# Kernel tuning notes

Hardware: AMD Instinct MI355X
Metric: run time of the kernel (lower is better)

The kernel has to match this reference:

```python
import jax, jax.numpy as jnp
import numpy as np

N, M, D, DV = 8192, 8192, 128, 128

def setup_inputs() -> dict:
    key = jax.random.key(0)
    kq, kk, kv = jax.random.split(key, 3)
    return {
        "Q": jax.random.normal(kq, (N, D), dtype=jnp.float32),
        "K": jax.random.normal(kk, (M, D), dtype=jnp.float32),
        "V": jax.random.normal(kv, (M, DV), dtype=jnp.float32),
    }

def reference(Q, K, V):
    # scores: [N, M] = Q @ K^T (no 1/sqrt(d) scaling, matching the source)
    scores = jnp.einsum("nd,md->nm", Q, K)
    attention_weights = jax.nn.softmax(scores, axis=1)  # softmax over keys
    return jnp.einsum("nm,mv->nv", attention_weights, V)  # [N, DV]
```

## Files before the change

kernel.cpp:

```cpp
#include <hip/hip_runtime.h>
#include <hip/hip_bf16.h>

#define NQ   8192
#define NKEY 8192
#define DH   128

#define BQ   128
#define BK   64
#define BUFB 32768
#define LOG2E 1.44269504088896340736f

typedef __attribute__((ext_vector_type(8)))  short    short8;
typedef __attribute__((ext_vector_type(4)))  short    short4v;
typedef _Float16 half8 __attribute__((ext_vector_type(8)));
typedef __attribute__((ext_vector_type(16))) float    f32x16;
typedef __attribute__((ext_vector_type(4)))  float    float4v;

union BFU { __hip_bfloat16 b; unsigned short u; };
__device__ __forceinline__ unsigned short f2bf(float x) { BFU u; u.b = __float2bfloat16(x); return u.u; }

__device__ __forceinline__ void full_drain_barrier() {
    __builtin_amdgcn_s_waitcnt(0);
    __syncthreads();
}

__global__ void prep(const float* __restrict__ K, const float* __restrict__ V,
                     _Float16* __restrict__ Kh, unsigned short* __restrict__ Vt) {
    __shared__ __attribute__((aligned(16))) unsigned short tile[64 * 72];
    int b = blockIdx.x;
    int t = threadIdx.x;
    if (b < 512) {
        int idx = (b * 256 + t) * 8;
        float4v x0 = *(const float4v*)(K + idx);
        float4v x1 = *(const float4v*)(K + idx + 4);
        half8 o;
#pragma unroll
        for (int j = 0; j < 4; ++j) { o[j] = (_Float16)x0[j]; o[4 + j] = (_Float16)x1[j]; }
        *(half8*)(Kh + idx) = o;
    } else {
        int tv = b - 512;
        int m0 = (tv >> 1) * 64, n0 = (tv & 1) * 64;
#pragma unroll
        for (int it = 0; it < 4; ++it) {
            int id = t + it * 256;
            int mm = id >> 4, nn0 = (id & 15) * 4;
            int mmP = (mm & ~12) | ((mm & 4) << 1) | ((mm & 8) >> 1);
            float4v x = *(const float4v*)(V + (size_t)(m0 + mm) * DH + n0 + nn0);
#pragma unroll
            for (int j = 0; j < 4; ++j)
                tile[(nn0 + j) * 72 + mmP] = f2bf(x[j]);
        }
        __syncthreads();
        int nn = t >> 2, ch = t & 3;
        *(short8*)(Vt + (size_t)(n0 + nn) * NKEY + m0 + ch * 16)     = *(const short8*)&tile[nn * 72 + ch * 16];
        *(short8*)(Vt + (size_t)(n0 + nn) * NKEY + m0 + ch * 16 + 8) = *(const short8*)&tile[nn * 72 + ch * 16 + 8];
    }
}

__launch_bounds__(256, 2)
__global__ void attn_fwd(const float* __restrict__ Q,
                         const _Float16* __restrict__ Kh,
                         const unsigned short* __restrict__ Vt,
                         unsigned short* __restrict__ Opart, float* __restrict__ lpart,
                         float* __restrict__ out, int KS) {
    __shared__ __attribute__((aligned(16))) char sbuf[2 * BUFB];

    const int tid  = threadIdx.x;
    const int lane = tid & 63;
    const int w    = tid >> 6;
    const int l31  = lane & 31;
    const int h    = lane >> 5;

    const int s  = blockIdx.x % KS;
    const int qb = blockIdx.x / KS;
    const int mlen   = NKEY / KS;
    const int kbase  = s * mlen;
    const int ntiles = mlen / BK;

    const char* gbase[8]; int mult[8]; int ldsoff[8];
#pragma unroll
    for (int i = 0; i < 8; ++i) {
        int Lb = w * 512 + i * 64;
        int L  = Lb + lane;
        const char* gb; int mu;
        if (Lb < 1024) { int r = L >> 4, cg = (L & 15) ^ (r & 15);
                         gb = (const char*)Kh + r * 256 + cg * 16; mu = 256; }
        else           { int Lv = L - 1024; int n = Lv >> 3, cg = (Lv & 7) ^ (n & 7);
                         gb = (const char*)Vt + (size_t)n * (NKEY * 2) + cg * 16; mu = 2; }
        gbase[i] = gb; mult[i] = mu; ldsoff[i] = Lb * 16;
    }

    const int qrow = qb * BQ + w * 32 + l31;
    half8 qf[8];
#pragma unroll
    for (int c = 0; c < 8; ++c) {
        const float* qp = Q + (size_t)qrow * DH + c * 16 + h * 8;
        float4v x0 = *(const float4v*)qp;
        float4v x1 = *(const float4v*)(qp + 4);
#pragma unroll
        for (int i = 0; i < 4; ++i) {
            qf[c][i]     = (_Float16)(x0[i] * LOG2E);
            qf[c][4 + i] = (_Float16)(x1[i] * LOG2E);
        }
    }

    int koff[8];
#pragma unroll
    for (int c = 0; c < 8; ++c)
        koff[c] = l31 * 256 + (((c * 2 + h) ^ (l31 & 15)) << 4);
    int voff[4];
#pragma unroll
    for (int c2 = 0; c2 < 4; ++c2)
        voff[c2] = 16384 + l31 * 128 + (((c2 * 2 + h) ^ (l31 & 7)) << 4);

    float lsum = 0.0f;
    f32x16 O[4];
#pragma unroll
    for (int ct = 0; ct < 4; ++ct)
#pragma unroll
        for (int r = 0; r < 16; ++r) O[ct][r] = 0.0f;

    auto stage = [&](int t, int bufbyte) {
        int kb = kbase + t * BK;
#pragma unroll
        for (int i = 0; i < 8; ++i) {
            const char* g = gbase[i] + (size_t)kb * mult[i];
            __builtin_amdgcn_global_load_lds(
                (const __attribute__((address_space(1))) unsigned int*)g,
                (__attribute__((address_space(3))) unsigned int*)(sbuf + bufbyte + ldsoff[i]),
                16, 0, 0);
        }
    };

    auto compute_tile = [&](int BUF) {
        const char* bp = sbuf + BUF;
        f32x16 S0, S1;
#pragma unroll
        for (int r = 0; r < 16; ++r) { S0[r] = 0.0f; S1[r] = 0.0f; }
#pragma unroll
        for (int c = 0; c < 8; ++c) {
            half8 k0 = *(const half8*)(bp + koff[c]);
            half8 k1 = *(const half8*)(bp + koff[c] + 8192);
            S0 = __builtin_amdgcn_mfma_f32_32x32x16_f16(k0, qf[c], S0, 0, 0, 0);
            S1 = __builtin_amdgcn_mfma_f32_32x32x16_f16(k1, qf[c], S1, 0, 0, 0);
        }
        union PU { unsigned int u[4]; short8 s8; } B0, B1, B2, B3;
        {
            float p0[16]; float ps = 0.0f;
#pragma unroll
            for (int r = 0; r < 16; ++r) { p0[r] = __builtin_amdgcn_exp2f(S0[r]); ps += p0[r]; }
            lsum += ps;
#pragma unroll
            for (int j = 0; j < 4; ++j) {
                B0.u[j] = __builtin_amdgcn_perm(__float_as_uint(p0[2*j+1]), __float_as_uint(p0[2*j]),   0x07060302u);
                B1.u[j] = __builtin_amdgcn_perm(__float_as_uint(p0[2*j+9]), __float_as_uint(p0[2*j+8]), 0x07060302u);
            }
#pragma unroll
            for (int ct = 0; ct < 4; ++ct) {
                short8 va0 = *(const short8*)(bp + voff[0] + ct * 4096);
                short8 va1 = *(const short8*)(bp + voff[1] + ct * 4096);
                O[ct] = __builtin_amdgcn_mfma_f32_32x32x16_bf16(va0, B0.s8, O[ct], 0, 0, 0);
                O[ct] = __builtin_amdgcn_mfma_f32_32x32x16_bf16(va1, B1.s8, O[ct], 0, 0, 0);
            }
        }
        {
            float p1[16]; float ps = 0.0f;
#pragma unroll
            for (int r = 0; r < 16; ++r) { p1[r] = __builtin_amdgcn_exp2f(S1[r]); ps += p1[r]; }
            lsum += ps;
#pragma unroll
            for (int j = 0; j < 4; ++j) {
                B2.u[j] = __builtin_amdgcn_perm(__float_as_uint(p1[2*j+1]), __float_as_uint(p1[2*j]),   0x07060302u);
                B3.u[j] = __builtin_amdgcn_perm(__float_as_uint(p1[2*j+9]), __float_as_uint(p1[2*j+8]), 0x07060302u);
            }
#pragma unroll
            for (int ct = 0; ct < 4; ++ct) {
                short8 va2 = *(const short8*)(bp + voff[2] + ct * 4096);
                short8 va3 = *(const short8*)(bp + voff[3] + ct * 4096);
                O[ct] = __builtin_amdgcn_mfma_f32_32x32x16_bf16(va2, B2.s8, O[ct], 0, 0, 0);
                O[ct] = __builtin_amdgcn_mfma_f32_32x32x16_bf16(va3, B3.s8, O[ct], 0, 0, 0);
            }
        }
    };

    stage(0, 0);
    for (int t = 0; t < ntiles; t += 2) {
        full_drain_barrier();
        stage(t + 1, BUFB);
        compute_tile(0);
        full_drain_barrier();
        if (t + 2 < ntiles) stage(t + 2, 0);
        compute_tile(BUFB);
    }

    lsum += __shfl_xor(lsum, 32, 64);
    {
        unsigned short* Ob = Opart + ((size_t)s * NQ + qrow) * DH;
#pragma unroll
        for (int ct = 0; ct < 4; ++ct)
#pragma unroll
            for (int g = 0; g < 4; ++g) {
                short4v v;
#pragma unroll
                for (int j = 0; j < 4; ++j) v[j] = (short)f2bf(O[ct][4 * g + j]);
                *(short4v*)(Ob + ct * 32 + 8 * g + 4 * h) = v;
            }
        if (h == 0)
            lpart[(size_t)s * NQ + qrow] = lsum;
    }
}

__global__ void attn_combine(const unsigned short* __restrict__ Opart,
                             const float* __restrict__ lpart, float* __restrict__ out, int KS) {
    int idx = blockIdx.x * 256 + threadIdx.x;
    int row = idx >> 5;
    int col = (idx & 31) << 2;
    float den = 0.0f;
    float a0 = 0.0f, a1 = 0.0f, a2 = 0.0f, a3 = 0.0f;
    for (int s2 = 0; s2 < KS; ++s2) {
        den += lpart[(size_t)s2 * NQ + row];
        const unsigned short* op = Opart + ((size_t)s2 * NQ + row) * DH + col;
        uint2 u = *(const uint2*)op;
        a0 += __uint_as_float(u.x << 16);
        a1 += __uint_as_float(u.x & 0xffff0000u);
        a2 += __uint_as_float(u.y << 16);
        a3 += __uint_as_float(u.y & 0xffff0000u);
    }
    float r = 1.0f / den;
    float4v v; v[0] = a0 * r; v[1] = a1 * r; v[2] = a2 * r; v[3] = a3 * r;
    *(float4v*)(out + (size_t)row * DH + col) = v;
}

extern "C" void kernel_launch(void* const* d_in, const int* in_sizes, int n_in,
                              void* d_out, int out_size, void* d_ws, size_t ws_size,
                              hipStream_t stream) {
    const float* Q = (const float*)d_in[0];
    const float* K = (const float*)d_in[1];
    const float* V = (const float*)d_in[2];
    float* out = (float*)d_out;

    const size_t prep_bytes = 2 * (size_t)NKEY * DH * sizeof(unsigned short);
    int KS = 8;
    while (KS > 1 &&
           ws_size < prep_bytes + (size_t)KS * ((size_t)NQ * DH * 2 + NQ * 4))
        KS >>= 1;

    _Float16* Kh = (_Float16*)d_ws;
    unsigned short* Vt = (unsigned short*)(Kh + (size_t)NKEY * DH);
    unsigned short* Opart = Vt + (size_t)NKEY * DH;
    float* lpart = (float*)(Opart + (size_t)KS * NQ * DH);

    hipLaunchKernelGGL(prep, dim3(768), dim3(256), 0, stream, K, V, Kh, Vt);
    hipLaunchKernelGGL(attn_fwd, dim3((NQ / BQ) * KS), dim3(256), 0, stream,
                       Q, Kh, Vt, Opart, lpart, out, KS);
    hipLaunchKernelGGL(attn_combine, dim3((NQ * DH) / 4 / 256), dim3(256), 0, stream,
                       Opart, lpart, out, KS);
}
```

Measured before the change: 113.7 us.

## Fuse split-K combine into attention kernel via last-block atomic counter

Drops the separate combine launch. Each attention block bumps a per-query-block atomic counter after writing its partial output, and the last of the KS split blocks reduces the partials and writes the final output. The prep kernel zeroes the counters. This removes one kernel launch and its scheduling gap, at the cost of a thread fence and an atomic per block, plus a serialized tail reduction done by only one block per query tile.

```diff
diff --git a/kernel.cpp b/kernel.cpp
--- a/kernel.cpp
+++ b/kernel.cpp
@@ -25,10 +25,12 @@
 }
 
 __global__ void prep(const float* __restrict__ K, const float* __restrict__ V,
-                     _Float16* __restrict__ Kh, unsigned short* __restrict__ Vt) {
+                     _Float16* __restrict__ Kh, unsigned short* __restrict__ Vt,
+                     int* __restrict__ cnt) {
     __shared__ __attribute__((aligned(16))) unsigned short tile[64 * 72];
     int b = blockIdx.x;
     int t = threadIdx.x;
+    if (b == 0 && t < 64) cnt[t] = 0;
     if (b < 512) {
         int idx = (b * 256 + t) * 8;
         float4v x0 = *(const float4v*)(K + idx);
@@ -62,7 +64,7 @@
                          const _Float16* __restrict__ Kh,
                          const unsigned short* __restrict__ Vt,
                          unsigned short* __restrict__ Opart, float* __restrict__ lpart,
-                         float* __restrict__ out, int KS) {
+                         int* __restrict__ cnt, float* __restrict__ out, int KS) {
     __shared__ __attribute__((aligned(16))) char sbuf[2 * BUFB];
 
     const int tid  = threadIdx.x;
@@ -208,27 +210,34 @@
         if (h == 0)
             lpart[(size_t)s * NQ + qrow] = lsum;
     }
-}
-
-__global__ void attn_combine(const unsigned short* __restrict__ Opart,
-                             const float* __restrict__ lpart, float* __restrict__ out, int KS) {
-    int idx = blockIdx.x * 256 + threadIdx.x;
-    int row = idx >> 5;
-    int col = (idx & 31) << 2;
-    float den = 0.0f;
-    float a0 = 0.0f, a1 = 0.0f, a2 = 0.0f, a3 = 0.0f;
-    for (int s2 = 0; s2 < KS; ++s2) {
-        den += lpart[(size_t)s2 * NQ + row];
-        const unsigned short* op = Opart + ((size_t)s2 * NQ + row) * DH + col;
-        uint2 u = *(const uint2*)op;
-        a0 += __uint_as_float(u.x << 16);
-        a1 += __uint_as_float(u.x & 0xffff0000u);
-        a2 += __uint_as_float(u.y << 16);
-        a3 += __uint_as_float(u.y & 0xffff0000u);
-    }
-    float r = 1.0f / den;
-    float4v v; v[0] = a0 * r; v[1] = a1 * r; v[2] = a2 * r; v[3] = a3 * r;
-    *(float4v*)(out + (size_t)row * DH + col) = v;
+
+    __shared__ int amLast;
+    __threadfence();
+    __syncthreads();
+    if (tid == 0)
+        amLast = (atomicAdd(&cnt[qb], 1) == KS - 1);
+    __syncthreads();
+    if (amLast) {
+        __threadfence();
+        const int rowbase = qb * BQ;
+        for (int c = tid; c < BQ * (DH / 4); c += 256) {
+            int row  = rowbase + (c >> 5);
+            int colq = (c & 31) << 2;
+            float den = 0.0f, a0 = 0.0f, a1 = 0.0f, a2 = 0.0f, a3 = 0.0f;
+            for (int s2 = 0; s2 < KS; ++s2) {
+                den += lpart[(size_t)s2 * NQ + row];
+                const unsigned short* op = Opart + ((size_t)s2 * NQ + row) * DH + colq;
+                uint2 u = *(const uint2*)op;
+                a0 += __uint_as_float(u.x << 16);
+                a1 += __uint_as_float(u.x & 0xffff0000u);
+                a2 += __uint_as_float(u.y << 16);
+                a3 += __uint_as_float(u.y & 0xffff0000u);
+            }
+            float r = 1.0f / den;
+            float4v v; v[0] = a0 * r; v[1] = a1 * r; v[2] = a2 * r; v[3] = a3 * r;
+            *(float4v*)(out + (size_t)row * DH + colq) = v;
+        }
+    }
 }
 
 extern "C" void kernel_launch(void* const* d_in, const int* in_sizes, int n_in,
@@ -242,17 +251,16 @@
     const size_t prep_bytes = 2 * (size_t)NKEY * DH * sizeof(unsigned short);
     int KS = 8;
     while (KS > 1 &&
-           ws_size < prep_bytes + (size_t)KS * ((size_t)NQ * DH * 2 + NQ * 4))
+           ws_size < prep_bytes + (size_t)KS * ((size_t)NQ * DH * 2 + NQ * 4) + 256)
         KS >>= 1;
 
     _Float16* Kh = (_Float16*)d_ws;
     unsigned short* Vt = (unsigned short*)(Kh + (size_t)NKEY * DH);
     unsigned short* Opart = Vt + (size_t)NKEY * DH;
     float* lpart = (float*)(Opart + (size_t)KS * NQ * DH);
-
-    hipLaunchKernelGGL(prep, dim3(768), dim3(256), 0, stream, K, V, Kh, Vt);
+    int* cnt = (int*)(lpart + (size_t)KS * NQ);
+
+    hipLaunchKernelGGL(prep, dim3(768), dim3(256), 0, stream, K, V, Kh, Vt, cnt);
     hipLaunchKernelGGL(attn_fwd, dim3((NQ / BQ) * KS), dim3(256), 0, stream,
-                       Q, Kh, Vt, Opart, lpart, out, KS);
-    hipLaunchKernelGGL(attn_combine, dim3((NQ * DH) / 4 / 256), dim3(256), 0, stream,
-                       Opart, lpart, out, KS);
-}
+                       Q, Kh, Vt, Opart, lpart, cnt, out, KS);
+}
```

After: 229.7 us. 102% more time.

## Load V operands directly from global into registers, stage only K in LDS

Applied to the files above, without the earlier changes.

V tiles are no longer staged through LDS. Each lane now loads its bf16 V fragments straight from global memory into registers at the start of each tile, and only K is staged via global_load_lds. This halves the LDS buffer size and removes the V LDS reads. The cost is that V global loads sit on the critical path right before the MFMAs, which can expose latency, and the issue order of the next stage now follows those loads.

```diff
diff --git a/kernel.cpp b/kernel.cpp
--- a/kernel.cpp
+++ b/kernel.cpp
@@ -7,7 +7,7 @@
 
 #define BQ   128
 #define BK   64
-#define BUFB 32768
+#define BUFB 16384
 #define LOG2E 1.44269504088896340736f
 
 typedef __attribute__((ext_vector_type(8)))  short    short8;
@@ -77,18 +77,20 @@
     const int kbase  = s * mlen;
     const int ntiles = mlen / BK;
 
-    const char* gbase[8]; int mult[8]; int ldsoff[8];
-#pragma unroll
-    for (int i = 0; i < 8; ++i) {
-        int Lb = w * 512 + i * 64;
+    const char* kgb[4]; int ldsoff[4];
+#pragma unroll
+    for (int i = 0; i < 4; ++i) {
+        int Lb = w * 256 + i * 64;
         int L  = Lb + lane;
-        const char* gb; int mu;
-        if (Lb < 1024) { int r = L >> 4, cg = (L & 15) ^ (r & 15);
-                         gb = (const char*)Kh + r * 256 + cg * 16; mu = 256; }
-        else           { int Lv = L - 1024; int n = Lv >> 3, cg = (Lv & 7) ^ (n & 7);
-                         gb = (const char*)Vt + (size_t)n * (NKEY * 2) + cg * 16; mu = 2; }
-        gbase[i] = gb; mult[i] = mu; ldsoff[i] = Lb * 16;
-    }
+        int r = L >> 4, ck = (L & 15) ^ (r & 15);
+        kgb[i] = (const char*)Kh + r * 256 + ck * 16;
+        ldsoff[i] = Lb * 16;
+    }
+
+    const char* vbase[4];
+#pragma unroll
+    for (int ct = 0; ct < 4; ++ct)
+        vbase[ct] = (const char*)Vt + (size_t)(ct * 32 + l31) * (NKEY * 2) + h * 16;
 
     const int qrow = qb * BQ + w * 32 + l31;
     half8 qf[8];
@@ -108,10 +110,6 @@
 #pragma unroll
     for (int c = 0; c < 8; ++c)
         koff[c] = l31 * 256 + (((c * 2 + h) ^ (l31 & 15)) << 4);
-    int voff[4];
-#pragma unroll
-    for (int c2 = 0; c2 < 4; ++c2)
-        voff[c2] = 16384 + l31 * 128 + (((c2 * 2 + h) ^ (l31 & 7)) << 4);
 
     float lsum = 0.0f;
     f32x16 O[4];
@@ -121,19 +119,25 @@
         for (int r = 0; r < 16; ++r) O[ct][r] = 0.0f;
 
     auto stage = [&](int t, int bufbyte) {
-        int kb = kbase + t * BK;
-#pragma unroll
-        for (int i = 0; i < 8; ++i) {
-            const char* g = gbase[i] + (size_t)kb * mult[i];
+        size_t gk = (size_t)(kbase + t * BK) * 256;
+#pragma unroll
+        for (int i = 0; i < 4; ++i)
             __builtin_amdgcn_global_load_lds(
-                (const __attribute__((address_space(1))) unsigned int*)g,
+                (const __attribute__((address_space(1))) unsigned int*)(kgb[i] + gk),
                 (__attribute__((address_space(3))) unsigned int*)(sbuf + bufbyte + ldsoff[i]),
                 16, 0, 0);
-        }
     };
 
-    auto compute_tile = [&](int BUF) {
+    auto compute_tile = [&](int BUF, int t, int tn, int nbuf) {
         const char* bp = sbuf + BUF;
+        const size_t kb2 = (size_t)(kbase + t * BK) * 2;
+        short8 va[4][4];
+#pragma unroll
+        for (int ct = 0; ct < 4; ++ct)
+#pragma unroll
+            for (int c2 = 0; c2 < 4; ++c2)
+                va[ct][c2] = *(const short8*)(vbase[ct] + kb2 + c2 * 32);
+        if (tn < ntiles) stage(tn, nbuf);
         f32x16 S0, S1;
 #pragma unroll
         for (int r = 0; r < 16; ++r) { S0[r] = 0.0f; S1[r] = 0.0f; }
@@ -157,10 +161,8 @@
             }
 #pragma unroll
             for (int ct = 0; ct < 4; ++ct) {
-                short8 va0 = *(const short8*)(bp + voff[0] + ct * 4096);
-                short8 va1 = *(const short8*)(bp + voff[1] + ct * 4096);
-                O[ct] = __builtin_amdgcn_mfma_f32_32x32x16_bf16(va0, B0.s8, O[ct], 0, 0, 0);
-                O[ct] = __builtin_amdgcn_mfma_f32_32x32x16_bf16(va1, B1.s8, O[ct], 0, 0, 0);
+                O[ct] = __builtin_amdgcn_mfma_f32_32x32x16_bf16(va[ct][0], B0.s8, O[ct], 0, 0, 0);
+                O[ct] = __builtin_amdgcn_mfma_f32_32x32x16_bf16(va[ct][1], B1.s8, O[ct], 0, 0, 0);
             }
         }
         {
@@ -175,10 +177,8 @@
             }
 #pragma unroll
             for (int ct = 0; ct < 4; ++ct) {
-                short8 va2 = *(const short8*)(bp + voff[2] + ct * 4096);
-                short8 va3 = *(const short8*)(bp + voff[3] + ct * 4096);
-                O[ct] = __builtin_amdgcn_mfma_f32_32x32x16_bf16(va2, B2.s8, O[ct], 0, 0, 0);
-                O[ct] = __builtin_amdgcn_mfma_f32_32x32x16_bf16(va3, B3.s8, O[ct], 0, 0, 0);
+                O[ct] = __builtin_amdgcn_mfma_f32_32x32x16_bf16(va[ct][2], B2.s8, O[ct], 0, 0, 0);
+                O[ct] = __builtin_amdgcn_mfma_f32_32x32x16_bf16(va[ct][3], B3.s8, O[ct], 0, 0, 0);
             }
         }
     };
@@ -186,11 +186,9 @@
     stage(0, 0);
     for (int t = 0; t < ntiles; t += 2) {
         full_drain_barrier();
-        stage(t + 1, BUFB);
-        compute_tile(0);
+        compute_tile(0, t, t + 1, BUFB);
         full_drain_barrier();
-        if (t + 2 < ntiles) stage(t + 2, 0);
-        compute_tile(BUFB);
+        compute_tile(BUFB, t + 1, t + 2, 0);
     }
 
     lsum += __shfl_xor(lsum, 32, 64);
```

After: 169.7 us. +49.3%, slower.
